# Performance work log

Hardware: AMD Instinct MI355X
Metric: run time of the kernel (lower is better)

Reference implementation:

```python
import jax, jax.numpy as jnp
import numpy as np

N = 1024        # num_entities
H_DIM = 128     # hidden_dim
HEADS = 8
C_HEAD = H_DIM // HEADS
LAYERS = 3
NEG = -1e9


def setup_inputs() -> dict:
    key = jax.random.key(0)
    ks = jax.random.split(key, 18)
    s = 0.02
    f = jnp.float32
    return {
        'mention_features': jax.random.normal(ks[0], (64, H_DIM), f),
        'mention_locations': jax.random.randint(ks[1], (64,), 0, N),
        'entity_embeddings': jax.random.normal(ks[2], (N, H_DIM), f),
        # edge predictor: Linear(2h,h) -> ReLU -> Linear(h,1) -> Sigmoid
        'W1': jax.random.normal(ks[3], (2 * H_DIM, H_DIM), f) * s,
        'b1': jnp.zeros((H_DIM,), f),
        'W2': jax.random.normal(ks[4], (H_DIM, 1), f) * s,
        'b2': jnp.zeros((1,), f),
        # per-layer TransformerConv params (stacked over LAYERS)
        'Wq': jax.random.normal(ks[5], (LAYERS, H_DIM, H_DIM), f) * s,
        'bq': jnp.zeros((LAYERS, H_DIM), f),
        'Wk': jax.random.normal(ks[6], (LAYERS, H_DIM, H_DIM), f) * s,
        'bk': jnp.zeros((LAYERS, H_DIM), f),
        'Wv': jax.random.normal(ks[7], (LAYERS, H_DIM, H_DIM), f) * s,
        'bv': jnp.zeros((LAYERS, H_DIM), f),
        'We': jax.random.normal(ks[8], (LAYERS, H_DIM), f) * s,   # lin_edge: 1 -> H*C, no bias
        'Ws': jax.random.normal(ks[9], (LAYERS, H_DIM, H_DIM), f) * s,  # root/skip linear
        'bs': jnp.zeros((LAYERS, H_DIM), f),
    }


def _edge_graph(x, W1, b1, W2, b2):
    # pair[i,j] = cat(x_i, x_j); split the cat-Linear to avoid [N,N,2h]
    a = x @ W1[:H_DIM]            # [N,h] (source i contribution)
    b = x @ W1[H_DIM:]            # [N,h] (target j contribution)
    h1 = jax.nn.relu(a[:, None, :] + b[None, :, :] + b1)   # [N,N,h]
    logits = jnp.einsum('ijh,h->ij', h1, W2[:, 0]) + b2[0]  # [N,N] indexed [source,target]
    w = jax.nn.sigmoid(logits)
    mask = logits > 0.0           # sigmoid(l) > 0.5  <=>  l > 0
    return w, mask


def _transformer_conv(x, w_st, mask_st, Wq, bq, Wk, bk, Wv, bv, We, Ws, bs):
    # PyG TransformerConv: edge (j=source -> i=target), scalar edge attr w[j,i]
    q = (x @ Wq + bq).reshape(N, HEADS, C_HEAD)
    k = (x @ Wk + bk).reshape(N, HEADS, C_HEAD)
    v = (x @ Wv + bv).reshape(N, HEADS, C_HEAD)
    We_hc = We.reshape(HEADS, C_HEAD)
    scale = 1.0 / jnp.sqrt(jnp.asarray(C_HEAD, x.dtype))
    w_ts = w_st.T                  # [target i, source j]
    m_ts = mask_st.T
    # alpha logits: q_i . (k_j + w_ji * We) / sqrt(C), rank-1 edge term decomposed
    logits = jnp.einsum('ihc,jhc->hij', q, k)              # [H,N,N]
    qWe = jnp.einsum('ihc,hc->ih', q, We_hc)               # [N,H]
    logits = (logits + qWe.T[:, :, None] * w_ts[None]) * scale
    logits = jnp.where(m_ts[None], logits, NEG)
    alpha = jax.nn.softmax(logits, axis=-1)
    alpha = alpha * m_ts[None]    # zero out rows with no incoming edges
    # out_i = sum_j alpha * (v_j + w_ji * We)
    out = jnp.einsum('hij,jhc->ihc', alpha, v)
    aw = jnp.einsum('hij,ij->ih', alpha, w_ts)
    out = out + aw[:, :, None] * We_hc[None]
    return out.reshape(N, H_DIM) + x @ Ws + bs


def reference(mention_features, mention_locations, entity_embeddings,
              W1, b1, W2, b2, Wq, bq, Wk, bk, Wv, bv, We, Ws, bs):
    x = entity_embeddings
    w, mask = _edge_graph(x, W1, b1, W2, b2)   # graph built once from initial features
    for l in range(LAYERS):
        x = x + _transformer_conv(x, w, mask, Wq[l], bq[l], Wk[l], bk[l],
                                  Wv[l], bv[l], We[l], Ws[l], bs[l])
    return x
```

## Files before the change

### kernel.cpp

```cpp
#include <hip/hip_runtime.h>
#include <math.h>

#define NN 1024
#define HD 128
#define NH 8
#define CH 16
#define NLAYERS 3

#define ALP 130
#define PBM 4
#define ABM 2
#define QSC 0.36067376022224085f

typedef __attribute__((ext_vector_type(8))) short short8;
typedef __attribute__((ext_vector_type(4))) float f32x4;

union FRG { uint4 u; short8 s; };

__device__ __forceinline__ float bf16_to_f32(unsigned short u) {
    union { unsigned int i; float f; } x; x.i = ((unsigned int)u) << 16; return x.f;
}
__device__ __forceinline__ unsigned short f32_to_bf16(float f) {
    union { float f; unsigned int i; } x; x.f = f;
    const unsigned int r = x.i + 0x7FFFu + ((x.i >> 16) & 1u);
    return (unsigned short)(r >> 16);
}
__device__ __forceinline__ unsigned int fbits(float f) {
    union { float f; unsigned int i; } x; x.f = f; return x.i;
}

__global__ __launch_bounds__(256) void k_edge_ab(
        const float* __restrict__ x, const float* __restrict__ W1,
        const float* __restrict__ b1, float* __restrict__ a, float* __restrict__ b,
        float* __restrict__ xout) {
    __shared__ float xt[HD][ABM];
    __shared__ float red[2][ABM][HD];
    const int r0 = blockIdx.x * ABM;
    const int cb = blockIdx.y;
    const int t  = threadIdx.x;
    {
        const float xv = x[(r0 + (t >> 7)) * HD + (t & 127)];
        xt[t & 127][t >> 7] = xv;
        if (cb == 0) xout[(r0 + (t >> 7)) * HD + (t & 127)] = xv;
    }
    __syncthreads();
    const int c = t & 127, g = t >> 7;
    const float* wp = W1 + cb * HD * HD + g * 64 * HD + c;
    const float* xp = &xt[g * 64][0];
    float a0 = 0.f, a1 = 0.f;
    #pragma unroll 8
    for (int kk = 0; kk < 64; ++kk) {
        const float wv = wp[kk * HD];
        const float2 xv = *(const float2*)&xp[kk * ABM];
        a0 = fmaf(xv.x, wv, a0);
        a1 = fmaf(xv.y, wv, a1);
    }
    red[g][0][c] = a0; red[g][1][c] = a1;
    __syncthreads();
    if (t < HD) {
        float* dst = cb ? b : a;
        const float bias = cb ? b1[t] : 0.f;
        #pragma unroll
        for (int r = 0; r < ABM; ++r)
            dst[(r0 + r) * HD + t] = red[0][r][t] + red[1][r][t] + bias;
    }
}

__global__ __launch_bounds__(256) void k_edge_w(
        const float* __restrict__ a, const float* __restrict__ bb,
        const float* __restrict__ W2, const float* __restrict__ b2,
        unsigned short* __restrict__ wm) {
    __shared__ float al[32][ALP];
    __shared__ float bl[16][HD];
    const int t = threadIdx.x;
    const int s0 = blockIdx.x * 32, t0 = blockIdx.y * 16;
    for (int ii = t; ii < 2048; ii += 256) {
        const int row = ii >> 6, col = (ii & 63) * 2;
        *(float2*)&al[row][col] = *(const float2*)&a[(s0 + row) * HD + col];
    }
    for (int ii = t; ii < 512; ii += 256) {
        const int row = ii >> 5, col = (ii & 31) * 4;
        *(float4*)&bl[row][col] = *(const float4*)&bb[(t0 + row) * HD + col];
    }
    __syncthreads();
    const int s = t & 31, tt = t >> 5;
    float acc0 = 0.f, acc1 = 0.f;
    #pragma unroll 2
    for (int h4 = 0; h4 < HD; h4 += 4) {
        const float4 w2 = *(const float4*)&W2[h4];
        const float2 avA = *(const float2*)&al[s][h4];
        const float2 avB = *(const float2*)&al[s][h4 + 2];
        const float4 b0v = *(const float4*)&bl[tt][h4];
        const float4 b1v = *(const float4*)&bl[tt + 8][h4];
        acc0 = fmaf(fmaxf(avA.x + b0v.x, 0.f), w2.x, acc0);
        acc0 = fmaf(fmaxf(avA.y + b0v.y, 0.f), w2.y, acc0);
        acc0 = fmaf(fmaxf(avB.x + b0v.z, 0.f), w2.z, acc0);
        acc0 = fmaf(fmaxf(avB.y + b0v.w, 0.f), w2.w, acc0);
        acc1 = fmaf(fmaxf(avA.x + b1v.x, 0.f), w2.x, acc1);
        acc1 = fmaf(fmaxf(avA.y + b1v.y, 0.f), w2.y, acc1);
        acc1 = fmaf(fmaxf(avB.x + b1v.z, 0.f), w2.z, acc1);
        acc1 = fmaf(fmaxf(avB.y + b1v.w, 0.f), w2.w, acc1);
    }
    const float bias = b2[0];
    const float l0 = acc0 + bias, l1 = acc1 + bias;
    const float w0 = 1.f / (1.f + __expf(-l0));
    const float w1 = 1.f / (1.f + __expf(-l1));
    wm[(t0 + tt    ) * NN + s0 + s] = f32_to_bf16((l0 > 0.f) ? w0 : -w0);
    wm[(t0 + tt + 8) * NN + s0 + s] = f32_to_bf16((l1 > 0.f) ? w1 : -w1);
}

__global__ __launch_bounds__(256) void k_proj(
        const float* __restrict__ x,
        const float* __restrict__ Wq, const float* __restrict__ bq,
        const float* __restrict__ Wk, const float* __restrict__ bk,
        const float* __restrict__ Wv, const float* __restrict__ bv,
        const float* __restrict__ Wsk, const float* __restrict__ bsk,
        unsigned short* __restrict__ qb, unsigned short* __restrict__ kb,
        unsigned short* __restrict__ vT, float* __restrict__ skip) {
    __shared__ float xt[HD][PBM];
    __shared__ float red[2][PBM][HD];
    const int r0 = blockIdx.x * PBM;
    const int cb = blockIdx.y;
    const int t  = threadIdx.x;
    {
        const int r = t >> 6, c2 = (t & 63) * 2;
        const float2 xv = *(const float2*)&x[(r0 + r) * HD + c2];
        xt[c2][r] = xv.x; xt[c2 + 1][r] = xv.y;
    }
    __syncthreads();
    const int c = t & 127, g = t >> 7;
    const float* W = (cb == 0) ? Wq : (cb == 1) ? Wk : (cb == 2) ? Wv : Wsk;
    const float* wp = W + g * 64 * HD + c;
    const float* xp = &xt[g * 64][0];
    float a0 = 0.f, a1 = 0.f, a2 = 0.f, a3 = 0.f;
    #pragma unroll 8
    for (int kk = 0; kk < 64; ++kk) {
        const float wv = wp[kk * HD];
        const float4 xv = *(const float4*)&xp[kk * PBM];
        a0 = fmaf(xv.x, wv, a0);
        a1 = fmaf(xv.y, wv, a1);
        a2 = fmaf(xv.z, wv, a2);
        a3 = fmaf(xv.w, wv, a3);
    }
    red[g][0][c] = a0; red[g][1][c] = a1; red[g][2][c] = a2; red[g][3][c] = a3;
    __syncthreads();
    if (t < HD) {
        const float* bptr = (cb == 0) ? bq : (cb == 1) ? bk : (cb == 2) ? bv : bsk;
        const float bias = bptr[t];
        const int h = t >> 4, ch = t & 15;
        #pragma unroll
        for (int r = 0; r < PBM; ++r) {
            const float val = red[0][r][t] + red[1][r][t] + bias;
            const int row = r0 + r;
            if (cb == 3) {
                skip[row * HD + t] = val;
            } else if (cb == 0) {
                qb[(h * NN + row) * CH + ch] = f32_to_bf16(val);
            } else if (cb == 1) {
                kb[(h * NN + row) * CH + ch] = f32_to_bf16(val);
            } else {
                vT[(h * CH + ch) * NN + row] = f32_to_bf16(val);
            }
        }
    }
}

__global__ __launch_bounds__(256) void k_attn(
        const unsigned short* __restrict__ qb, const unsigned short* __restrict__ kb,
        const unsigned short* __restrict__ vT, const float* __restrict__ skip,
        const unsigned short* __restrict__ wm, const float* __restrict__ We,
        float* __restrict__ x) {
    __shared__ float mrg[4][16][20];
    const int i0 = blockIdx.x * 16;
    const int h  = blockIdx.y;
    const int t  = threadIdx.x;
    const int w  = t >> 6, l = t & 63;
    const int li = l & 15, G = l >> 4;

    FRG qf;
    if (G < 2) qf.u = *(const uint4*)(qb + ((size_t)h * NN + i0 + li) * CH + 8 * G);
    else       qf.u = make_uint4(0, 0, 0, 0);

    float qe = 0.f;
    {
        const uint4 qa = *(const uint4*)(qb + ((size_t)h * NN + i0 + li) * CH);
        const uint4 qb2 = *(const uint4*)(qb + ((size_t)h * NN + i0 + li) * CH + 8);
        const unsigned int qd[8] = {qa.x, qa.y, qa.z, qa.w, qb2.x, qb2.y, qb2.z, qb2.w};
        #pragma unroll
        for (int d2 = 0; d2 < 8; ++d2) {
            qe = fmaf(bf16_to_f32((unsigned short)(qd[d2] & 0xffff)), We[h * CH + 2 * d2], qe);
            qe = fmaf(bf16_to_f32((unsigned short)(qd[d2] >> 16)),    We[h * CH + 2 * d2 + 1], qe);
        }
        qe *= QSC;
    }
    const unsigned short* wrow = wm + (size_t)(i0 + li) * NN;
    const int j0s = w * 256;

    float m = -1e30f;
    float sst[16][4];
    #pragma unroll
    for (int tt = 0; tt < 16; ++tt) {
        const int j0 = j0s + tt * 16;
        FRG kf;
        if (G < 2) kf.u = *(const uint4*)(kb + ((size_t)h * NN + j0 + li) * CH + 8 * G);
        else       kf.u = make_uint4(0, 0, 0, 0);
        f32x4 d = __builtin_amdgcn_mfma_f32_16x16x32_bf16(kf.s, qf.s, (f32x4){0.f, 0.f, 0.f, 0.f}, 0, 0, 0);
        const uint2 wmu = *(const uint2*)(wrow + j0 + 4 * G);
        const unsigned short wu[4] = {(unsigned short)(wmu.x & 0xffff), (unsigned short)(wmu.x >> 16),
                                      (unsigned short)(wmu.y & 0xffff), (unsigned short)(wmu.y >> 16)};
        #pragma unroll
        for (int rg = 0; rg < 4; ++rg) {
            const float wv = bf16_to_f32(wu[rg]);
            const float sv = (wv > 0.f) ? fmaf(qe, wv, d[rg] * QSC) : -1e30f;
            sst[tt][rg] = sv;
            m = fmaxf(m, sv);
        }
    }
    m = fmaxf(m, __shfl_xor(m, 16));
    m = fmaxf(m, __shfl_xor(m, 32));

    f32x4 oc = {0.f, 0.f, 0.f, 0.f};
    float sum = 0.f, aw = 0.f;
    const int srcA = (G & 1) * 32 + li;
    const int srcB = srcA + 16;
    #pragma unroll
    for (int cc = 0; cc < 8; ++cc) {
        unsigned int pk[4];
        #pragma unroll
        for (int hh = 0; hh < 2; ++hh) {
            const int tt = 2 * cc + hh;
            const uint2 wmu = *(const uint2*)(wrow + j0s + tt * 16 + 4 * G);
            const unsigned short wu[4] = {(unsigned short)(wmu.x & 0xffff), (unsigned short)(wmu.x >> 16),
                                          (unsigned short)(wmu.y & 0xffff), (unsigned short)(wmu.y >> 16)};
            float p[4];
            #pragma unroll
            for (int rg = 0; rg < 4; ++rg) {
                p[rg] = __builtin_amdgcn_exp2f(sst[tt][rg] - m);
                sum += p[rg];
                aw = fmaf(p[rg], fabsf(bf16_to_f32(wu[rg])), aw);
            }
            pk[2 * hh]     = (fbits(p[0]) >> 16) | (fbits(p[1]) & 0xffff0000u);
            pk[2 * hh + 1] = (fbits(p[2]) >> 16) | (fbits(p[3]) & 0xffff0000u);
        }
        const unsigned int a0 = (unsigned int)__shfl((int)pk[0], srcA);
        const unsigned int a1 = (unsigned int)__shfl((int)pk[1], srcA);
        const unsigned int a2 = (unsigned int)__shfl((int)pk[0], srcB);
        const unsigned int a3 = (unsigned int)__shfl((int)pk[1], srcB);
        const unsigned int b0 = (unsigned int)__shfl((int)pk[2], srcA);
        const unsigned int b1 = (unsigned int)__shfl((int)pk[3], srcA);
        const unsigned int b2 = (unsigned int)__shfl((int)pk[2], srcB);
        const unsigned int b3 = (unsigned int)__shfl((int)pk[3], srcB);
        FRG pf;
        pf.u.x = (G >= 2) ? b0 : a0;
        pf.u.y = (G >= 2) ? b1 : a1;
        pf.u.z = (G >= 2) ? b2 : a2;
        pf.u.w = (G >= 2) ? b3 : a3;
        FRG vf;
        vf.u = *(const uint4*)(vT + ((size_t)h * CH + li) * NN + j0s + cc * 32 + 8 * G);
        oc = __builtin_amdgcn_mfma_f32_16x16x32_bf16(pf.s, vf.s, oc, 0, 0, 0);
    }
    sum += __shfl_xor(sum, 16); sum += __shfl_xor(sum, 32);
    aw  += __shfl_xor(aw, 16);  aw  += __shfl_xor(aw, 32);

    if (l < 16) { mrg[w][l][0] = m; mrg[w][l][1] = sum; mrg[w][l][2] = aw; }
    #pragma unroll
    for (int rg = 0; rg < 4; ++rg) mrg[w][4 * G + rg][3 + li] = oc[rg];
    __syncthreads();

    {
        const int r2 = t >> 4, c = t & 15;
        const float m0 = mrg[0][r2][0], m1 = mrg[1][r2][0], m2 = mrg[2][r2][0], m3 = mrg[3][r2][0];
        const float ms = fmaxf(fmaxf(m0, m1), fmaxf(m2, m3));
        const float f0 = __builtin_amdgcn_exp2f(m0 - ms);
        const float f1 = __builtin_amdgcn_exp2f(m1 - ms);
        const float f2 = __builtin_amdgcn_exp2f(m2 - ms);
        const float f3 = __builtin_amdgcn_exp2f(m3 - ms);
        const float sums = f0 * mrg[0][r2][1] + f1 * mrg[1][r2][1] + f2 * mrg[2][r2][1] + f3 * mrg[3][r2][1];
        const float aws  = f0 * mrg[0][r2][2] + f1 * mrg[1][r2][2] + f2 * mrg[2][r2][2] + f3 * mrg[3][r2][2];
        const float ocm  = f0 * mrg[0][r2][3 + c] + f1 * mrg[1][r2][3 + c]
                         + f2 * mrg[2][r2][3 + c] + f3 * mrg[3][r2][3 + c];
        const float inv = (ms > -1e29f) ? 1.f / sums : 0.f;
        const int idx = (i0 + r2) * HD + h * CH + c;
        x[idx] = x[idx] + skip[idx] + ocm * inv + (aws * inv) * We[h * CH + c];
    }
}

extern "C" void kernel_launch(void* const* d_in, const int* in_sizes, int n_in,
                              void* d_out, int out_size, void* d_ws, size_t ws_size,
                              hipStream_t stream) {
    const float* ent = (const float*)d_in[2];
    const float* W1  = (const float*)d_in[3];
    const float* b1  = (const float*)d_in[4];
    const float* W2  = (const float*)d_in[5];
    const float* b2  = (const float*)d_in[6];
    const float* Wq  = (const float*)d_in[7];
    const float* bq  = (const float*)d_in[8];
    const float* Wk  = (const float*)d_in[9];
    const float* bk  = (const float*)d_in[10];
    const float* Wv  = (const float*)d_in[11];
    const float* bv  = (const float*)d_in[12];
    const float* We  = (const float*)d_in[13];
    const float* Ws  = (const float*)d_in[14];
    const float* bs  = (const float*)d_in[15];

    unsigned short* wm = (unsigned short*)d_ws;
    float* a  = (float*)(wm + (size_t)NN * NN);
    float* bf = a + NN * HD;
    float* sk = bf + NN * HD;
    unsigned short* qb = (unsigned short*)(sk + NN * HD);
    unsigned short* kb = qb + NN * HD;
    unsigned short* vT = kb + NN * HD;
    float* x  = (float*)d_out;

    k_edge_ab<<<dim3(NN / ABM, 2), 256, 0, stream>>>(ent, W1, b1, a, bf, x);
    k_edge_w<<<dim3(32, 64), 256, 0, stream>>>(a, bf, W2, b2, wm);

    for (int l = 0; l < NLAYERS; ++l) {
        k_proj<<<dim3(NN / PBM, 4), 256, 0, stream>>>(x,
            Wq + l * HD * HD, bq + l * HD, Wk + l * HD * HD, bk + l * HD,
            Wv + l * HD * HD, bv + l * HD, Ws + l * HD * HD, bs + l * HD,
            qb, kb, vT, sk);
        k_attn<<<dim3(NN / 16, NH), 256, 0, stream>>>(qb, kb, vT, sk, wm, We + l * HD, x);
    }
}
```

Before: 82.29 us.

## Split attention key range across eight waves and pack edge MLP math

The attention kernel now runs 512 threads per block, so each of eight waves handles 128 keys instead of 256. The per-wave softmax partials are merged across all eight in shared memory. This halves per-thread register state (the sst array) and the serial loop length, aiming to improve latency hiding, at the cost of a larger merge step. Separately, the edge-weight kernel now uses 2-wide float vector FMA/max ops, which may map to packed FP32 instructions.

```diff
diff --git a/kernel.cpp b/kernel.cpp
--- a/kernel.cpp
+++ b/kernel.cpp
@@ -14,6 +14,7 @@
 
 typedef __attribute__((ext_vector_type(8))) short short8;
 typedef __attribute__((ext_vector_type(4))) float f32x4;
+typedef __attribute__((ext_vector_type(2))) float f32x2;
 
 union FRG { uint4 u; short8 s; };
 
@@ -84,25 +85,25 @@
     }
     __syncthreads();
     const int s = t & 31, tt = t >> 5;
-    float acc0 = 0.f, acc1 = 0.f;
+    const f32x2 zz = {0.f, 0.f};
+    f32x2 acc0 = zz, acc1 = zz;
     #pragma unroll 2
     for (int h4 = 0; h4 < HD; h4 += 4) {
-        const float4 w2 = *(const float4*)&W2[h4];
-        const float2 avA = *(const float2*)&al[s][h4];
-        const float2 avB = *(const float2*)&al[s][h4 + 2];
-        const float4 b0v = *(const float4*)&bl[tt][h4];
-        const float4 b1v = *(const float4*)&bl[tt + 8][h4];
-        acc0 = fmaf(fmaxf(avA.x + b0v.x, 0.f), w2.x, acc0);
-        acc0 = fmaf(fmaxf(avA.y + b0v.y, 0.f), w2.y, acc0);
-        acc0 = fmaf(fmaxf(avB.x + b0v.z, 0.f), w2.z, acc0);
-        acc0 = fmaf(fmaxf(avB.y + b0v.w, 0.f), w2.w, acc0);
-        acc1 = fmaf(fmaxf(avA.x + b1v.x, 0.f), w2.x, acc1);
-        acc1 = fmaf(fmaxf(avA.y + b1v.y, 0.f), w2.y, acc1);
-        acc1 = fmaf(fmaxf(avB.x + b1v.z, 0.f), w2.z, acc1);
-        acc1 = fmaf(fmaxf(avB.y + b1v.w, 0.f), w2.w, acc1);
+        const f32x2 w2a = {W2[h4],     W2[h4 + 1]};
+        const f32x2 w2b = {W2[h4 + 2], W2[h4 + 3]};
+        const f32x2 avA = *(const f32x2*)&al[s][h4];
+        const f32x2 avB = *(const f32x2*)&al[s][h4 + 2];
+        const f32x2 b0a = *(const f32x2*)&bl[tt][h4];
+        const f32x2 b0b = *(const f32x2*)&bl[tt][h4 + 2];
+        const f32x2 b1a = *(const f32x2*)&bl[tt + 8][h4];
+        const f32x2 b1b = *(const f32x2*)&bl[tt + 8][h4 + 2];
+        acc0 = __builtin_elementwise_fma(__builtin_elementwise_max(avA + b0a, zz), w2a, acc0);
+        acc0 = __builtin_elementwise_fma(__builtin_elementwise_max(avB + b0b, zz), w2b, acc0);
+        acc1 = __builtin_elementwise_fma(__builtin_elementwise_max(avA + b1a, zz), w2a, acc1);
+        acc1 = __builtin_elementwise_fma(__builtin_elementwise_max(avB + b1b, zz), w2b, acc1);
     }
     const float bias = b2[0];
-    const float l0 = acc0 + bias, l1 = acc1 + bias;
+    const float l0 = acc0.x + acc0.y + bias, l1 = acc1.x + acc1.y + bias;
     const float w0 = 1.f / (1.f + __expf(-l0));
     const float w1 = 1.f / (1.f + __expf(-l1));
     wm[(t0 + tt    ) * NN + s0 + s] = f32_to_bf16((l0 > 0.f) ? w0 : -w0);
@@ -165,12 +166,12 @@
     }
 }
 
-__global__ __launch_bounds__(256) void k_attn(
+__global__ __launch_bounds__(512) void k_attn(
         const unsigned short* __restrict__ qb, const unsigned short* __restrict__ kb,
         const unsigned short* __restrict__ vT, const float* __restrict__ skip,
         const unsigned short* __restrict__ wm, const float* __restrict__ We,
         float* __restrict__ x) {
-    __shared__ float mrg[4][16][20];
+    __shared__ float mrg[8][16][20];
     const int i0 = blockIdx.x * 16;
     const int h  = blockIdx.y;
     const int t  = threadIdx.x;
@@ -194,12 +195,12 @@
         qe *= QSC;
     }
     const unsigned short* wrow = wm + (size_t)(i0 + li) * NN;
-    const int j0s = w * 256;
+    const int j0s = w * 128;
 
     float m = -1e30f;
-    float sst[16][4];
+    float sst[8][4];
     #pragma unroll
-    for (int tt = 0; tt < 16; ++tt) {
+    for (int tt = 0; tt < 8; ++tt) {
         const int j0 = j0s + tt * 16;
         FRG kf;
         if (G < 2) kf.u = *(const uint4*)(kb + ((size_t)h * NN + j0 + li) * CH + 8 * G);
@@ -224,7 +225,7 @@
     const int srcA = (G & 1) * 32 + li;
     const int srcB = srcA + 16;
     #pragma unroll
-    for (int cc = 0; cc < 8; ++cc) {
+    for (int cc = 0; cc < 4; ++cc) {
         unsigned int pk[4];
         #pragma unroll
         for (int hh = 0; hh < 2; ++hh) {
@@ -267,18 +268,19 @@
     for (int rg = 0; rg < 4; ++rg) mrg[w][4 * G + rg][3 + li] = oc[rg];
     __syncthreads();
 
-    {
+    if (t < 256) {
         const int r2 = t >> 4, c = t & 15;
-        const float m0 = mrg[0][r2][0], m1 = mrg[1][r2][0], m2 = mrg[2][r2][0], m3 = mrg[3][r2][0];
-        const float ms = fmaxf(fmaxf(m0, m1), fmaxf(m2, m3));
-        const float f0 = __builtin_amdgcn_exp2f(m0 - ms);
-        const float f1 = __builtin_amdgcn_exp2f(m1 - ms);
-        const float f2 = __builtin_amdgcn_exp2f(m2 - ms);
-        const float f3 = __builtin_amdgcn_exp2f(m3 - ms);
-        const float sums = f0 * mrg[0][r2][1] + f1 * mrg[1][r2][1] + f2 * mrg[2][r2][1] + f3 * mrg[3][r2][1];
-        const float aws  = f0 * mrg[0][r2][2] + f1 * mrg[1][r2][2] + f2 * mrg[2][r2][2] + f3 * mrg[3][r2][2];
-        const float ocm  = f0 * mrg[0][r2][3 + c] + f1 * mrg[1][r2][3 + c]
-                         + f2 * mrg[2][r2][3 + c] + f3 * mrg[3][r2][3 + c];
+        float ms = -1e30f;
+        #pragma unroll
+        for (int k = 0; k < 8; ++k) ms = fmaxf(ms, mrg[k][r2][0]);
+        float sums = 0.f, aws = 0.f, ocm = 0.f;
+        #pragma unroll
+        for (int k = 0; k < 8; ++k) {
+            const float fk = __builtin_amdgcn_exp2f(mrg[k][r2][0] - ms);
+            sums = fmaf(fk, mrg[k][r2][1], sums);
+            aws  = fmaf(fk, mrg[k][r2][2], aws);
+            ocm  = fmaf(fk, mrg[k][r2][3 + c], ocm);
+        }
         const float inv = (ms > -1e29f) ? 1.f / sums : 0.f;
         const int idx = (i0 + r2) * HD + h * CH + c;
         x[idx] = x[idx] + skip[idx] + ocm * inv + (aws * inv) * We[h * CH + c];
@@ -320,6 +322,6 @@
             Wq + l * HD * HD, bq + l * HD, Wk + l * HD * HD, bk + l * HD,
             Wv + l * HD * HD, bv + l * HD, Ws + l * HD * HD, bs + l * HD,
             qb, kb, vT, sk);
-        k_attn<<<dim3(NN / 16, NH), 256, 0, stream>>>(qb, kb, vT, sk, wm, We + l * HD, x);
-    }
-}
+        k_attn<<<dim3(NN / 16, NH), 512, 0, stream>>>(qb, kb, vT, sk, wm, We + l * HD, x);
+    }
+}
```

Result: faster. 78.45 us, median of 2 (-4.7%).
